# Performance work log

Hardware: AMD Instinct MI355X
Metric: run time of the kernel (lower is better)

## Reference

```python
import jax, jax.numpy as jnp
import numpy as np

B, H, W, C = 1, 56, 56, 96
DI = 192          # d_inner = ssm_ratio * hidden_dim
N  = 16           # d_state
DR = 6            # dt_rank = ceil(96/16)
K  = 4            # cross-scan directions
MH = 384          # mlp hidden = 4*C
L  = H * W


def _ln(x, g, b):
    m = x.mean(-1, keepdims=True)
    v = ((x - m) ** 2).mean(-1, keepdims=True)
    return (x - m) * jax.lax.rsqrt(v + 1e-5) * g + b


def setup_inputs() -> dict:
    key = jax.random.key(0)
    ks = jax.random.split(key, 12)
    r = lambda i, shape, s=0.02: jax.random.normal(ks[i], shape, jnp.float32) * s
    # S4D-real init for A_logs: log(1..N) tiled over K*DI channels
    A_logs = jnp.log(jnp.tile(jnp.arange(1, N + 1, dtype=jnp.float32)[None, :], (K * DI, 1)))
    return dict(
        x=jax.random.normal(ks[0], (B, H, W, C), jnp.float32),
        norm_g=jnp.ones((C,)), norm_b=jnp.zeros((C,)),
        in_proj_w=r(1, (C, 2 * DI)),
        conv_w=r(2, (3, 3, 1, DI)), conv_b=jnp.zeros((DI,)),
        x_proj_w=r(3, (K, DR + 2 * N, DI)),
        dt_projs_w=r(4, (K, DI, DR), 0.1), dt_projs_b=r(5, (K, DI), 0.1),
        A_logs=A_logs, Ds=jnp.ones((K * DI,)),
        out_norm_g=jnp.ones((DI,)), out_norm_b=jnp.zeros((DI,)),
        out_proj_w=r(6, (DI, C)),
        norm2_g=jnp.ones((C,)), norm2_b=jnp.zeros((C,)),
        fc1_w=r(7, (C, MH)), fc1_b=jnp.zeros((MH,)),
        fc2_w=r(8, (MH, C)), fc2_b=jnp.zeros((C,)),
    )


def _ss2d(x, in_proj_w, conv_w, conv_b, x_proj_w, dt_projs_w, dt_projs_b,
          A_logs, Ds, out_norm_g, out_norm_b, out_proj_w):
    xz = x @ in_proj_w                                  # (B,H,W,2*DI)
    xx, z = xz[..., :DI], xz[..., DI:]
    z = jax.nn.silu(z)
    xx = jax.lax.conv_general_dilated(
        xx, conv_w, (1, 1), 'SAME',
        dimension_numbers=('NHWC', 'HWIO', 'NHWC'),
        feature_group_count=DI) + conv_b               # depthwise 3x3
    xx = jax.nn.silu(xx)
    # cross-scan: row-major, col-major, and their reverses -> (B,K,DI,L)
    xd = jnp.transpose(xx, (0, 3, 1, 2)).reshape(B, DI, L)
    xt = jnp.transpose(xx, (0, 3, 2, 1)).reshape(B, DI, L)
    xs = jnp.stack([xd, xt, xd[..., ::-1], xt[..., ::-1]], 1)
    xdbl = jnp.einsum('bkdl,kcd->bkcl', xs, x_proj_w)
    dts, Bs, Cs = xdbl[:, :, :DR], xdbl[:, :, DR:DR + N], xdbl[:, :, DR + N:]
    dts = jnp.einsum('bkrl,kdr->bkdl', dts, dt_projs_w)
    dts = jax.nn.softplus(dts + dt_projs_b[None, :, :, None])      # (B,K,DI,L)
    A = -jnp.exp(A_logs).reshape(K, DI, N)
    # selective scan as first-order linear recurrence h_t = a_t*h_{t-1} + b_t
    a = jnp.exp(dts[..., None] * A[None, :, :, None, :])           # (B,K,DI,L,N)
    b = dts[..., None] * jnp.swapaxes(Bs, -1, -2)[:, :, None] * xs[..., None]
    def comb(c1, c2):
        a1, b1 = c1
        a2, b2 = c2
        return a1 * a2, a2 * b1 + b2
    _, hs = jax.lax.associative_scan(comb, (a, b), axis=3)         # (B,K,DI,L,N)
    ys = jnp.einsum('bkdln,bknl->bkdl', hs, Cs) + Ds.reshape(K, DI)[None, :, :, None] * xs
    # cross-merge: un-flip, un-transpose, sum the 4 directions
    yrow = ys[:, 0] + ys[:, 2, :, ::-1]
    ycol = ys[:, 1] + ys[:, 3, :, ::-1]
    y = yrow + jnp.transpose(ycol.reshape(B, DI, W, H), (0, 1, 3, 2)).reshape(B, DI, L)
    y = jnp.transpose(y.reshape(B, DI, H, W), (0, 2, 3, 1))        # (B,H,W,DI)
    y = _ln(y, out_norm_g, out_norm_b) * z
    return y @ out_proj_w


def reference(x, norm_g, norm_b, in_proj_w, conv_w, conv_b, x_proj_w,
              dt_projs_w, dt_projs_b, A_logs, Ds, out_norm_g, out_norm_b,
              out_proj_w, norm2_g, norm2_b, fc1_w, fc1_b, fc2_w, fc2_b):
    x = x + _ss2d(_ln(x, norm_g, norm_b), in_proj_w, conv_w, conv_b, x_proj_w,
                  dt_projs_w, dt_projs_b, A_logs, Ds, out_norm_g, out_norm_b, out_proj_w)
    h = _ln(x, norm2_g, norm2_b)
    x = x + (jax.nn.gelu(h @ fc1_w + fc1_b) @ fc2_w + fc2_b)
    return x
```

## Files before the change

### kernel.cpp

```cpp
#include <hip/hip_runtime.h>
#include <math.h>

constexpr int cH = 56, cW = 56, cC = 96, cDI = 192, cN = 16, cDR = 6, cK = 4, cMH = 384;
constexpr int cL = cH * cW;
constexpr int cNC = 49;
constexpr int cCH = 64;
constexpr float LOG2E = 1.44269504088896340736f;

__device__ __forceinline__ float fast_exp2(float x) { return __builtin_amdgcn_exp2f(x); }
__device__ __forceinline__ float siluf(float x) { return x / (1.f + expf(-x)); }
__device__ __forceinline__ float geluf(float x) {
    float x3 = x * x * x;
    return 0.5f * x * (1.f + tanhf(0.7978845608028654f * (x + 0.044715f * x3)));
}

__device__ __forceinline__ float dpp_red16(float v) {
    union { float f; int i; } u, r;
    u.f = v; r.i = __builtin_amdgcn_update_dpp(0, u.i, 0xB1, 0xF, 0xF, true);  v += r.f;
    u.f = v; r.i = __builtin_amdgcn_update_dpp(0, u.i, 0x4E, 0xF, 0xF, true);  v += r.f;
    u.f = v; r.i = __builtin_amdgcn_update_dpp(0, u.i, 0x141, 0xF, 0xF, true); v += r.f;
    u.f = v; r.i = __builtin_amdgcn_update_dpp(0, u.i, 0x140, 0xF, 0xF, true); v += r.f;
    return v;
}

__global__ void ln96_kernel(const float* __restrict__ x, const float* __restrict__ g,
                            const float* __restrict__ b, float* __restrict__ out, int M) {
    int wid = threadIdx.x >> 6;
    int lane = threadIdx.x & 63;
    int row = blockIdx.x * 4 + wid;
    if (row >= M) return;
    const float* xr = x + row * cC;
    float v0 = xr[lane];
    float v1 = (lane < cC - 64) ? xr[lane + 64] : 0.f;
    float s = v0 + v1;
    float sq = v0 * v0 + v1 * v1;
#pragma unroll
    for (int off = 32; off; off >>= 1) {
        s += __shfl_xor(s, off, 64);
        sq += __shfl_xor(sq, off, 64);
    }
    float m = s * (1.f / cC);
    float var = sq * (1.f / cC) - m * m;
    float rstd = rsqrtf(var + 1e-5f);
    out[row * cC + lane] = (v0 - m) * rstd * g[lane] + b[lane];
    if (lane < cC - 64)
        out[row * cC + lane + 64] = (v1 - m) * rstd * g[lane + 64] + b[lane + 64];
}

template <int ACT, bool HASB, bool HASR>
__global__ __launch_bounds__(256) void gemm_tile_kernel(
    const float* __restrict__ A, const float* __restrict__ B,
    const float* __restrict__ bias, const float* __restrict__ res,
    float* __restrict__ C, int M, int Nn, int Kk) {
    __shared__ float As[64][36];
    __shared__ float Bs[32][32];
    int tid = threadIdx.x;
    int tx = tid & 15;
    int ty = tid >> 4;
    int row0 = blockIdx.y * 64;
    int n0 = blockIdx.x * 32;
    float acc[4][2] = {{0.f, 0.f}, {0.f, 0.f}, {0.f, 0.f}, {0.f, 0.f}};
    int nt = Kk >> 5;
    for (int kt = 0; kt < nt; kt++) {
#pragma unroll
        for (int t = 0; t < 2; t++) {
            int f = tid + t * 256;
            int ar = f >> 3, ac = (f & 7) * 4;
            const float4 v = *reinterpret_cast<const float4*>(
                A + (size_t)(row0 + ar) * Kk + kt * 32 + ac);
            *reinterpret_cast<float4*>(&As[ar][ac]) = v;
        }
        {
            int br = tid >> 3, bc = (tid & 7) * 4;
            const float4 v = *reinterpret_cast<const float4*>(
                B + (size_t)(kt * 32 + br) * Nn + n0 + bc);
            *reinterpret_cast<float4*>(&Bs[br][bc]) = v;
        }
        __syncthreads();
#pragma unroll
        for (int k4 = 0; k4 < 8; k4++) {
            float4 a0 = *reinterpret_cast<float4*>(&As[ty * 4 + 0][k4 * 4]);
            float4 a1 = *reinterpret_cast<float4*>(&As[ty * 4 + 1][k4 * 4]);
            float4 a2 = *reinterpret_cast<float4*>(&As[ty * 4 + 2][k4 * 4]);
            float4 a3 = *reinterpret_cast<float4*>(&As[ty * 4 + 3][k4 * 4]);
            float2 b0 = *reinterpret_cast<float2*>(&Bs[k4 * 4 + 0][tx * 2]);
            float2 b1 = *reinterpret_cast<float2*>(&Bs[k4 * 4 + 1][tx * 2]);
            float2 b2 = *reinterpret_cast<float2*>(&Bs[k4 * 4 + 2][tx * 2]);
            float2 b3 = *reinterpret_cast<float2*>(&Bs[k4 * 4 + 3][tx * 2]);
            acc[0][0] = fmaf(a0.x, b0.x, acc[0][0]); acc[0][1] = fmaf(a0.x, b0.y, acc[0][1]);
            acc[1][0] = fmaf(a1.x, b0.x, acc[1][0]); acc[1][1] = fmaf(a1.x, b0.y, acc[1][1]);
            acc[2][0] = fmaf(a2.x, b0.x, acc[2][0]); acc[2][1] = fmaf(a2.x, b0.y, acc[2][1]);
            acc[3][0] = fmaf(a3.x, b0.x, acc[3][0]); acc[3][1] = fmaf(a3.x, b0.y, acc[3][1]);
            acc[0][0] = fmaf(a0.y, b1.x, acc[0][0]); acc[0][1] = fmaf(a0.y, b1.y, acc[0][1]);
            acc[1][0] = fmaf(a1.y, b1.x, acc[1][0]); acc[1][1] = fmaf(a1.y, b1.y, acc[1][1]);
            acc[2][0] = fmaf(a2.y, b1.x, acc[2][0]); acc[2][1] = fmaf(a2.y, b1.y, acc[2][1]);
            acc[3][0] = fmaf(a3.y, b1.x, acc[3][0]); acc[3][1] = fmaf(a3.y, b1.y, acc[3][1]);
            acc[0][0] = fmaf(a0.z, b2.x, acc[0][0]); acc[0][1] = fmaf(a0.z, b2.y, acc[0][1]);
            acc[1][0] = fmaf(a1.z, b2.x, acc[1][0]); acc[1][1] = fmaf(a1.z, b2.y, acc[1][1]);
            acc[2][0] = fmaf(a2.z, b2.x, acc[2][0]); acc[2][1] = fmaf(a2.z, b2.y, acc[2][1]);
            acc[3][0] = fmaf(a3.z, b2.x, acc[3][0]); acc[3][1] = fmaf(a3.z, b2.y, acc[3][1]);
            acc[0][0] = fmaf(a0.w, b3.x, acc[0][0]); acc[0][1] = fmaf(a0.w, b3.y, acc[0][1]);
            acc[1][0] = fmaf(a1.w, b3.x, acc[1][0]); acc[1][1] = fmaf(a1.w, b3.y, acc[1][1]);
            acc[2][0] = fmaf(a2.w, b3.x, acc[2][0]); acc[2][1] = fmaf(a2.w, b3.y, acc[2][1]);
            acc[3][0] = fmaf(a3.w, b3.x, acc[3][0]); acc[3][1] = fmaf(a3.w, b3.y, acc[3][1]);
        }
        __syncthreads();
    }
    int cc = n0 + tx * 2;
    float bx_ = 0.f, by_ = 0.f;
    if (HASB) { bx_ = bias[cc]; by_ = bias[cc + 1]; }
#pragma unroll
    for (int i = 0; i < 4; i++) {
        int rr = row0 + ty * 4 + i;
        float v0 = acc[i][0], v1 = acc[i][1];
        if (HASB) { v0 += bx_; v1 += by_; }
        if (ACT == 1) { v0 = geluf(v0); v1 = geluf(v1); }
        if (HASR) {
            const float2 r2 = *reinterpret_cast<const float2*>(res + (size_t)rr * Nn + cc);
            v0 += r2.x; v1 += r2.y;
        }
        float2 o; o.x = v0; o.y = v1;
        *reinterpret_cast<float2*>(C + (size_t)rr * Nn + cc) = o;
    }
}

__global__ void conv_silu_kernel(const float* __restrict__ xz, const float* __restrict__ cw,
                                 const float* __restrict__ cb, float* __restrict__ out) {
    int idx = blockIdx.x * 256 + threadIdx.x;
    if (idx >= cL * cDI) return;
    int d = idx % cDI;
    int l = idx / cDI;
    int h = l / cW, w = l % cW;
    float s = cb[d];
#pragma unroll
    for (int dh = 0; dh < 3; dh++) {
        int hh = h + dh - 1;
        if (hh < 0 || hh >= cH) continue;
#pragma unroll
        for (int dw = 0; dw < 3; dw++) {
            int w2 = w + dw - 1;
            if (w2 < 0 || w2 >= cW) continue;
            s = fmaf(xz[(size_t)(hh * cW + w2) * (2 * cDI) + d], cw[(dh * 3 + dw) * cDI + d], s);
        }
    }
    out[idx] = siluf(s);
}

__global__ void proj_kernel(const float* __restrict__ xconv, const float* __restrict__ xpw,
                            const float* __restrict__ dtw, const float* __restrict__ dtb,
                            float* __restrict__ dtout, float* __restrict__ Bsout,
                            float* __restrict__ Csout) {
    __shared__ float XS[16 * 193];
    __shared__ float DTS[6 * 16];
    int k = blockIdx.y;
    int p0 = blockIdx.x * 16;
    int tid = threadIdx.x;
    for (int idx = tid; idx < 16 * cDI; idx += 256) {
        int p = idx / cDI, d = idx % cDI;
        int j = p0 + p;
        int jj = (k >= 2) ? (cL - 1 - j) : j;
        int rrow = (k & 1) ? ((jj % cH) * cW + (jj / cH)) : jj;
        XS[p * 193 + d] = xconv[(size_t)rrow * cDI + d];
    }
    __syncthreads();
    for (int o = tid; o < 38 * 16; o += 256) {
        int c = o >> 4, p = o & 15;
        const float* wr = xpw + (size_t)(k * 38 + c) * cDI;
        const float* xr = XS + p * 193;
        float s = 0.f;
#pragma unroll 4
        for (int d = 0; d < cDI; d++) s = fmaf(wr[d], xr[d], s);
        if (c < 6) DTS[c * 16 + p] = s;
        else if (c < 22) Bsout[(size_t)(k * cL + p0 + p) * cN + (c - 6)] = s;
        else Csout[(size_t)(k * cL + p0 + p) * cN + (c - 22)] = s;
    }
    __syncthreads();
    for (int o = tid; o < cDI * 16; o += 256) {
        int d = o >> 4, p = o & 15;
        float s = dtb[k * cDI + d];
        const float* wr = dtw + (size_t)(k * cDI + d) * cDR;
#pragma unroll
        for (int r = 0; r < cDR; r++) s = fmaf(wr[r], DTS[r * 16 + p], s);
        float sp = (s > 20.f) ? s : log1pf(expf(s));
        dtout[(size_t)(k * cDI + d) * cL + p0 + p] = sp;
    }
}

__device__ __forceinline__ void walker_init(int k, int j0, int& r, int& dr) {
    if (k == 0) { r = j0; dr = 1; }
    else if (k == 1) { r = (j0 % cH) * cW + (j0 / cH); dr = cW; }
    else if (k == 2) { r = cL - 1 - j0; dr = -1; }
    else { int jp = cL - 1 - j0; r = (jp % cH) * cW + (jp / cH); dr = -cW; }
}
__device__ __forceinline__ void walker_step(int& r, int dr) {
    r += dr;
    if (r >= cL) r -= cL - 1;
    else if (r < 0) r += cL - 1;
}

__global__ void scan1_kernel(const float* __restrict__ dtbuf, const float* __restrict__ Bs,
                             const float* __restrict__ xconv, const float* __restrict__ Alogs,
                             float* __restrict__ carryP, float* __restrict__ carryH) {
    int bx = blockIdx.x;
    int c = bx % cNC;
    int t2 = bx / cNC;
    int d0 = (t2 % (cDI / 16)) * 16;
    int k = t2 / (cDI / 16);
    int g = threadIdx.x >> 4;
    int n = threadIdx.x & 15;
    int d = d0 + g;
    int kd = k * cDI + d;
    float An2 = -expf(Alogs[kd * cN + n]) * LOG2E;
    int j0 = c * cCH;
    int r, dr;
    walker_init(k, j0, r, dr);
    const float* dtp = dtbuf + (size_t)kd * cL;
    const float* bsp = Bs + (size_t)k * cL * cN + n;
    float h = 0.f, S = 0.f;
    for (int i = 0; i < cCH; i += 4) {
        int j = j0 + i;
        const float4 dt4 = *reinterpret_cast<const float4*>(dtp + j);
        float xv0 = xconv[r * cDI + d]; walker_step(r, dr);
        float xv1 = xconv[r * cDI + d]; walker_step(r, dr);
        float xv2 = xconv[r * cDI + d]; walker_step(r, dr);
        float xv3 = xconv[r * cDI + d]; walker_step(r, dr);
        float bv0 = bsp[(size_t)(j + 0) * cN];
        float bv1 = bsp[(size_t)(j + 1) * cN];
        float bv2 = bsp[(size_t)(j + 2) * cN];
        float bv3 = bsp[(size_t)(j + 3) * cN];
        float a0 = fast_exp2(An2 * dt4.x);
        float a1 = fast_exp2(An2 * dt4.y);
        float a2 = fast_exp2(An2 * dt4.z);
        float a3 = fast_exp2(An2 * dt4.w);
        h = fmaf(a0, h, dt4.x * bv0 * xv0);
        h = fmaf(a1, h, dt4.y * bv1 * xv1);
        h = fmaf(a2, h, dt4.z * bv2 * xv2);
        h = fmaf(a3, h, dt4.w * bv3 * xv3);
        S += dt4.x + dt4.y + dt4.z + dt4.w;
    }
    float P = fast_exp2(An2 * S);
    int idxc = (kd * cNC + c) * cN + n;
    carryH[idxc] = h;
    carryP[idxc] = P;
}

__global__ void scan2_kernel(const float* __restrict__ carryP, const float* __restrict__ carryH,
                             float* __restrict__ hin) {
    int gid = blockIdx.x * 256 + threadIdx.x;
    if (gid >= cK * cDI * cN) return;
    int kd = gid / cN, n = gid % cN;
    float h = 0.f;
    for (int c = 0; c < cNC; c++) {
        int idxc = (kd * cNC + c) * cN + n;
        hin[idxc] = h;
        h = fmaf(carryP[idxc], h, carryH[idxc]);
    }
}

__global__ void scan3_kernel(const float* __restrict__ dtbuf, const float* __restrict__ Bs,
                             const float* __restrict__ Cs, const float* __restrict__ xconv,
                             const float* __restrict__ Alogs, const float* __restrict__ Ds,
                             const float* __restrict__ hin, float* __restrict__ ysS) {
    int bx = blockIdx.x;
    int c = bx % cNC;
    int t2 = bx / cNC;
    int d0 = (t2 % (cDI / 16)) * 16;
    int k = t2 / (cDI / 16);
    int g = threadIdx.x >> 4;
    int n = threadIdx.x & 15;
    int d = d0 + g;
    int kd = k * cDI + d;
    float An2 = -expf(Alogs[kd * cN + n]) * LOG2E;
    float Dv = Ds[kd];
    int j0 = c * cCH;
    int r, dr;
    walker_init(k, j0, r, dr);
    const float* dtp = dtbuf + (size_t)kd * cL;
    const float* bsp = Bs + (size_t)k * cL * cN + n;
    const float* csp = Cs + (size_t)k * cL * cN + n;
    float h = hin[(kd * cNC + c) * cN + n];
    for (int i = 0; i < cCH; i += 4) {
        int j = j0 + i;
        const float4 dt4 = *reinterpret_cast<const float4*>(dtp + j);
        float xv0 = xconv[r * cDI + d]; walker_step(r, dr);
        float xv1 = xconv[r * cDI + d]; walker_step(r, dr);
        float xv2 = xconv[r * cDI + d]; walker_step(r, dr);
        float xv3 = xconv[r * cDI + d]; walker_step(r, dr);
        float bv0 = bsp[(size_t)(j + 0) * cN];
        float bv1 = bsp[(size_t)(j + 1) * cN];
        float bv2 = bsp[(size_t)(j + 2) * cN];
        float bv3 = bsp[(size_t)(j + 3) * cN];
        float cv0 = csp[(size_t)(j + 0) * cN];
        float cv1 = csp[(size_t)(j + 1) * cN];
        float cv2 = csp[(size_t)(j + 2) * cN];
        float cv3 = csp[(size_t)(j + 3) * cN];
        float a0 = fast_exp2(An2 * dt4.x);
        float a1 = fast_exp2(An2 * dt4.y);
        float a2 = fast_exp2(An2 * dt4.z);
        float a3 = fast_exp2(An2 * dt4.w);
        h = fmaf(a0, h, dt4.x * bv0 * xv0);
        float t0 = dpp_red16(h * cv0);
        h = fmaf(a1, h, dt4.y * bv1 * xv1);
        float t1 = dpp_red16(h * cv1);
        h = fmaf(a2, h, dt4.z * bv2 * xv2);
        float t2v = dpp_red16(h * cv2);
        h = fmaf(a3, h, dt4.w * bv3 * xv3);
        float t3 = dpp_red16(h * cv3);
        if (n == 0) {
            ysS[(size_t)(k * cL + j + 0) * cDI + d] = t0 + Dv * xv0;
            ysS[(size_t)(k * cL + j + 1) * cDI + d] = t1 + Dv * xv1;
            ysS[(size_t)(k * cL + j + 2) * cDI + d] = t2v + Dv * xv2;
            ysS[(size_t)(k * cL + j + 3) * cDI + d] = t3 + Dv * xv3;
        }
    }
}

__global__ void lnout_kernel(const float* __restrict__ ysS, const float* __restrict__ xz,
                             const float* __restrict__ g, const float* __restrict__ b,
                             float* __restrict__ ymul) {
    int wid = threadIdx.x >> 6, lane = threadIdx.x & 63;
    int l = blockIdx.x * 4 + wid;
    if (l >= cL) return;
    int h_ = l / cW, w_ = l % cW;
    int lc = w_ * cH + h_;
    float v[3];
    float s = 0.f, sq = 0.f;
#pragma unroll
    for (int j = 0; j < 3; j++) {
        int d = lane + j * 64;
        float t = ysS[(size_t)(0 * cL + l) * cDI + d] +
                  ysS[(size_t)(1 * cL + lc) * cDI + d] +
                  ysS[(size_t)(2 * cL + (cL - 1 - l)) * cDI + d] +
                  ysS[(size_t)(3 * cL + (cL - 1 - lc)) * cDI + d];
        v[j] = t;
        s += t;
        sq += t * t;
    }
#pragma unroll
    for (int off = 32; off; off >>= 1) {
        s += __shfl_xor(s, off, 64);
        sq += __shfl_xor(sq, off, 64);
    }
    float m = s * (1.f / cDI);
    float var = sq * (1.f / cDI) - m * m;
    float rstd = rsqrtf(var + 1e-5f);
#pragma unroll
    for (int j = 0; j < 3; j++) {
        int d = lane + j * 64;
        float z = xz[(size_t)l * (2 * cDI) + cDI + d];
        ymul[(size_t)l * cDI + d] = ((v[j] - m) * rstd * g[d] + b[d]) * siluf(z);
    }
}

extern "C" void kernel_launch(void* const* d_in, const int* in_sizes, int n_in,
                              void* d_out, int out_size, void* d_ws, size_t ws_size,
                              hipStream_t stream) {
    const float* x         = (const float*)d_in[0];
    const float* norm_g    = (const float*)d_in[1];
    const float* norm_b    = (const float*)d_in[2];
    const float* in_proj_w = (const float*)d_in[3];
    const float* conv_w    = (const float*)d_in[4];
    const float* conv_b    = (const float*)d_in[5];
    const float* x_proj_w  = (const float*)d_in[6];
    const float* dt_projs_w= (const float*)d_in[7];
    const float* dt_projs_b= (const float*)d_in[8];
    const float* A_logs    = (const float*)d_in[9];
    const float* Ds        = (const float*)d_in[10];
    const float* out_norm_g= (const float*)d_in[11];
    const float* out_norm_b= (const float*)d_in[12];
    const float* out_proj_w= (const float*)d_in[13];
    const float* norm2_g   = (const float*)d_in[14];
    const float* norm2_b   = (const float*)d_in[15];
    const float* fc1_w     = (const float*)d_in[16];
    const float* fc1_b     = (const float*)d_in[17];
    const float* fc2_w     = (const float*)d_in[18];
    const float* fc2_b     = (const float*)d_in[19];

    float* ws = (float*)d_ws;
    float* ln_buf = ws;
    float* xz     = ws + 301056;
    float* xconv  = ws + 1505280;
    float* dtb_   = ws + 2107392;
    float* Bs     = ws + 4515840;
    float* Cs     = ws + 4716544;
    float* hin    = ws + 4917248;
    float* ysS    = ws + 5519360;
    float* cP     = ysS;
    float* cHh    = ysS + 602112;
    float* ymul   = xconv;
    float* x1     = ws + 7927808;
    float* hm     = xz;
    float* out    = (float*)d_out;

    ln96_kernel<<<cL / 4, 256, 0, stream>>>(x, norm_g, norm_b, ln_buf, cL);
    gemm_tile_kernel<0, false, false><<<dim3(384 / 32, cL / 64), 256, 0, stream>>>(
        ln_buf, in_proj_w, nullptr, nullptr, xz, cL, 2 * cDI, cC);
    conv_silu_kernel<<<(cL * cDI) / 256, 256, 0, stream>>>(xz, conv_w, conv_b, xconv);
    proj_kernel<<<dim3(cL / 16, cK), 256, 0, stream>>>(xconv, x_proj_w, dt_projs_w,
                                                       dt_projs_b, dtb_, Bs, Cs);
    scan1_kernel<<<cK * (cDI / 16) * cNC, 256, 0, stream>>>(dtb_, Bs, xconv, A_logs, cP, cHh);
    scan2_kernel<<<(cK * cDI * cN + 255) / 256, 256, 0, stream>>>(cP, cHh, hin);
    scan3_kernel<<<cK * (cDI / 16) * cNC, 256, 0, stream>>>(dtb_, Bs, Cs, xconv, A_logs, Ds,
                                                            hin, ysS);
    lnout_kernel<<<cL / 4, 256, 0, stream>>>(ysS, xz, out_norm_g, out_norm_b, ymul);
    gemm_tile_kernel<0, false, true><<<dim3(96 / 32, cL / 64), 256, 0, stream>>>(
        ymul, out_proj_w, nullptr, x, x1, cL, cC, cDI);
    ln96_kernel<<<cL / 4, 256, 0, stream>>>(x1, norm2_g, norm2_b, ln_buf, cL);
    gemm_tile_kernel<1, true, false><<<dim3(384 / 32, cL / 64), 256, 0, stream>>>(
        ln_buf, fc1_w, fc1_b, nullptr, hm, cL, cMH, cC);
    gemm_tile_kernel<0, true, true><<<dim3(96 / 32, cL / 64), 256, 0, stream>>>(
        hm, fc2_w, fc2_b, x1, out, cL, cC, cMH);
}
```

Before: 162.4 us.

## Restructure selective scan to one thread per channel with all states in registers

The scan kernels change from 16 lanes per channel (one per state, with a DPP reduction over C) to one thread per channel that keeps all 16 states in registers and accumulates y locally. B and C per chunk are staged in shared memory, dt is stored transposed (position-major) so loads across channels coalesce, and dt_projs weights are cached in LDS in proj_kernel. Chunk length drops from 64 to 16, giving 196 chunks so the grid stays large, at the cost of a longer sequential carry pass in scan2 and larger carry buffers. The workspace is re-laid out so the carry buffers no longer alias ysS.

```diff
diff --git a/kernel.cpp b/kernel.cpp
--- a/kernel.cpp
+++ b/kernel.cpp
@@ -3,8 +3,8 @@
 
 constexpr int cH = 56, cW = 56, cC = 96, cDI = 192, cN = 16, cDR = 6, cK = 4, cMH = 384;
 constexpr int cL = cH * cW;
-constexpr int cNC = 49;
-constexpr int cCH = 64;
+constexpr int cNC = 196;
+constexpr int cCH = 16;
 constexpr float LOG2E = 1.44269504088896340736f;
 
 __device__ __forceinline__ float fast_exp2(float x) { return __builtin_amdgcn_exp2f(x); }
@@ -12,15 +12,6 @@
 __device__ __forceinline__ float geluf(float x) {
     float x3 = x * x * x;
     return 0.5f * x * (1.f + tanhf(0.7978845608028654f * (x + 0.044715f * x3)));
-}
-
-__device__ __forceinline__ float dpp_red16(float v) {
-    union { float f; int i; } u, r;
-    u.f = v; r.i = __builtin_amdgcn_update_dpp(0, u.i, 0xB1, 0xF, 0xF, true);  v += r.f;
-    u.f = v; r.i = __builtin_amdgcn_update_dpp(0, u.i, 0x4E, 0xF, 0xF, true);  v += r.f;
-    u.f = v; r.i = __builtin_amdgcn_update_dpp(0, u.i, 0x141, 0xF, 0xF, true); v += r.f;
-    u.f = v; r.i = __builtin_amdgcn_update_dpp(0, u.i, 0x140, 0xF, 0xF, true); v += r.f;
-    return v;
 }
 
 __global__ void ln96_kernel(const float* __restrict__ x, const float* __restrict__ g,
@@ -148,13 +139,15 @@
 
 __global__ void proj_kernel(const float* __restrict__ xconv, const float* __restrict__ xpw,
                             const float* __restrict__ dtw, const float* __restrict__ dtb,
-                            float* __restrict__ dtout, float* __restrict__ Bsout,
+                            float* __restrict__ dtT, float* __restrict__ Bsout,
                             float* __restrict__ Csout) {
     __shared__ float XS[16 * 193];
     __shared__ float DTS[6 * 16];
+    __shared__ float DTW[cDI * cDR];
     int k = blockIdx.y;
     int p0 = blockIdx.x * 16;
     int tid = threadIdx.x;
+    for (int i = tid; i < cDI * cDR; i += 256) DTW[i] = dtw[k * cDI * cDR + i];
     for (int idx = tid; idx < 16 * cDI; idx += 256) {
         int p = idx / cDI, d = idx % cDI;
         int j = p0 + p;
@@ -176,13 +169,12 @@
     }
     __syncthreads();
     for (int o = tid; o < cDI * 16; o += 256) {
-        int d = o >> 4, p = o & 15;
+        int d = o % cDI, p = o / cDI;
         float s = dtb[k * cDI + d];
-        const float* wr = dtw + (size_t)(k * cDI + d) * cDR;
-#pragma unroll
-        for (int r = 0; r < cDR; r++) s = fmaf(wr[r], DTS[r * 16 + p], s);
+#pragma unroll
+        for (int r = 0; r < cDR; r++) s = fmaf(DTW[d * cDR + r], DTS[r * 16 + p], s);
         float sp = (s > 20.f) ? s : log1pf(expf(s));
-        dtout[(size_t)(k * cDI + d) * cL + p0 + p] = sp;
+        dtT[(size_t)(k * cL + p0 + p) * cDI + d] = sp;
     }
 }
 
@@ -198,50 +190,54 @@
     else if (r < 0) r += cL - 1;
 }
 
-__global__ void scan1_kernel(const float* __restrict__ dtbuf, const float* __restrict__ Bs,
-                             const float* __restrict__ xconv, const float* __restrict__ Alogs,
-                             float* __restrict__ carryP, float* __restrict__ carryH) {
-    int bx = blockIdx.x;
-    int c = bx % cNC;
-    int t2 = bx / cNC;
-    int d0 = (t2 % (cDI / 16)) * 16;
-    int k = t2 / (cDI / 16);
-    int g = threadIdx.x >> 4;
-    int n = threadIdx.x & 15;
-    int d = d0 + g;
+__global__ __launch_bounds__(192) void scan1_kernel(
+    const float* __restrict__ dtT, const float* __restrict__ Bs,
+    const float* __restrict__ xconv, const float* __restrict__ Alogs,
+    float* __restrict__ carryP, float* __restrict__ carryH) {
+    int c = blockIdx.x % cNC;
+    int k = blockIdx.x / cNC;
+    int d = threadIdx.x;
     int kd = k * cDI + d;
-    float An2 = -expf(Alogs[kd * cN + n]) * LOG2E;
     int j0 = c * cCH;
+    __shared__ float BS[cCH * cN];
+    for (int i = threadIdx.x; i < cCH * cN; i += 192)
+        BS[i] = Bs[(size_t)(k * cL + j0) * cN + i];
+    float An2[cN];
+#pragma unroll
+    for (int n = 0; n < cN; n++)
+        An2[n] = -fast_exp2(Alogs[kd * cN + n] * LOG2E) * LOG2E;
     int r, dr;
     walker_init(k, j0, r, dr);
-    const float* dtp = dtbuf + (size_t)kd * cL;
-    const float* bsp = Bs + (size_t)k * cL * cN + n;
-    float h = 0.f, S = 0.f;
-    for (int i = 0; i < cCH; i += 4) {
-        int j = j0 + i;
-        const float4 dt4 = *reinterpret_cast<const float4*>(dtp + j);
-        float xv0 = xconv[r * cDI + d]; walker_step(r, dr);
-        float xv1 = xconv[r * cDI + d]; walker_step(r, dr);
-        float xv2 = xconv[r * cDI + d]; walker_step(r, dr);
-        float xv3 = xconv[r * cDI + d]; walker_step(r, dr);
-        float bv0 = bsp[(size_t)(j + 0) * cN];
-        float bv1 = bsp[(size_t)(j + 1) * cN];
-        float bv2 = bsp[(size_t)(j + 2) * cN];
-        float bv3 = bsp[(size_t)(j + 3) * cN];
-        float a0 = fast_exp2(An2 * dt4.x);
-        float a1 = fast_exp2(An2 * dt4.y);
-        float a2 = fast_exp2(An2 * dt4.z);
-        float a3 = fast_exp2(An2 * dt4.w);
-        h = fmaf(a0, h, dt4.x * bv0 * xv0);
-        h = fmaf(a1, h, dt4.y * bv1 * xv1);
-        h = fmaf(a2, h, dt4.z * bv2 * xv2);
-        h = fmaf(a3, h, dt4.w * bv3 * xv3);
-        S += dt4.x + dt4.y + dt4.z + dt4.w;
-    }
-    float P = fast_exp2(An2 * S);
-    int idxc = (kd * cNC + c) * cN + n;
-    carryH[idxc] = h;
-    carryP[idxc] = P;
+    __syncthreads();
+    float h[cN];
+#pragma unroll
+    for (int n = 0; n < cN; n++) h[n] = 0.f;
+    float S = 0.f;
+    const float* dtp = dtT + (size_t)(k * cL + j0) * cDI + d;
+    for (int i = 0; i < cCH; i++) {
+        float dt = dtp[(size_t)i * cDI];
+        float xv = xconv[r * cDI + d];
+        walker_step(r, dr);
+        float dtx = dt * xv;
+        S += dt;
+        const float4 b0 = *reinterpret_cast<const float4*>(&BS[i * cN + 0]);
+        const float4 b1 = *reinterpret_cast<const float4*>(&BS[i * cN + 4]);
+        const float4 b2 = *reinterpret_cast<const float4*>(&BS[i * cN + 8]);
+        const float4 b3 = *reinterpret_cast<const float4*>(&BS[i * cN + 12]);
+        float bb[cN] = {b0.x, b0.y, b0.z, b0.w, b1.x, b1.y, b1.z, b1.w,
+                        b2.x, b2.y, b2.z, b2.w, b3.x, b3.y, b3.z, b3.w};
+#pragma unroll
+        for (int n = 0; n < cN; n++) {
+            float a = fast_exp2(An2[n] * dt);
+            h[n] = fmaf(a, h[n], bb[n] * dtx);
+        }
+    }
+    size_t cb = (size_t)(kd * cNC + c) * cN;
+#pragma unroll
+    for (int n = 0; n < cN; n++) {
+        carryH[cb + n] = h[n];
+        carryP[cb + n] = fast_exp2(An2[n] * S);
+    }
 }
 
 __global__ void scan2_kernel(const float* __restrict__ carryP, const float* __restrict__ carryH,
@@ -251,67 +247,76 @@
     int kd = gid / cN, n = gid % cN;
     float h = 0.f;
     for (int c = 0; c < cNC; c++) {
-        int idxc = (kd * cNC + c) * cN + n;
+        size_t idxc = (size_t)(kd * cNC + c) * cN + n;
         hin[idxc] = h;
         h = fmaf(carryP[idxc], h, carryH[idxc]);
     }
 }
 
-__global__ void scan3_kernel(const float* __restrict__ dtbuf, const float* __restrict__ Bs,
-                             const float* __restrict__ Cs, const float* __restrict__ xconv,
-                             const float* __restrict__ Alogs, const float* __restrict__ Ds,
-                             const float* __restrict__ hin, float* __restrict__ ysS) {
-    int bx = blockIdx.x;
-    int c = bx % cNC;
-    int t2 = bx / cNC;
-    int d0 = (t2 % (cDI / 16)) * 16;
-    int k = t2 / (cDI / 16);
-    int g = threadIdx.x >> 4;
-    int n = threadIdx.x & 15;
-    int d = d0 + g;
+__global__ __launch_bounds__(192) void scan3_kernel(
+    const float* __restrict__ dtT, const float* __restrict__ Bs,
+    const float* __restrict__ Cs, const float* __restrict__ xconv,
+    const float* __restrict__ Alogs, const float* __restrict__ Ds,
+    const float* __restrict__ hin, float* __restrict__ ysS) {
+    int c = blockIdx.x % cNC;
+    int k = blockIdx.x / cNC;
+    int d = threadIdx.x;
     int kd = k * cDI + d;
-    float An2 = -expf(Alogs[kd * cN + n]) * LOG2E;
+    int j0 = c * cCH;
+    __shared__ float BS[cCH * cN];
+    __shared__ float CS[cCH * cN];
+    for (int i = threadIdx.x; i < cCH * cN; i += 192) {
+        BS[i] = Bs[(size_t)(k * cL + j0) * cN + i];
+        CS[i] = Cs[(size_t)(k * cL + j0) * cN + i];
+    }
+    float An2[cN];
+#pragma unroll
+    for (int n = 0; n < cN; n++)
+        An2[n] = -fast_exp2(Alogs[kd * cN + n] * LOG2E) * LOG2E;
     float Dv = Ds[kd];
-    int j0 = c * cCH;
     int r, dr;
     walker_init(k, j0, r, dr);
-    const float* dtp = dtbuf + (size_t)kd * cL;
-    const float* bsp = Bs + (size_t)k * cL * cN + n;
-    const float* csp = Cs + (size_t)k * cL * cN + n;
-    float h = hin[(kd * cNC + c) * cN + n];
-    for (int i = 0; i < cCH; i += 4) {
-        int j = j0 + i;
-        const float4 dt4 = *reinterpret_cast<const float4*>(dtp + j);
-        float xv0 = xconv[r * cDI + d]; walker_step(r, dr);
-        float xv1 = xconv[r * cDI + d]; walker_step(r, dr);
-        float xv2 = xconv[r * cDI + d]; walker_step(r, dr);
-        float xv3 = xconv[r * cDI + d]; walker_step(r, dr);
-        float bv0 = bsp[(size_t)(j + 0) * cN];
-        float bv1 = bsp[(size_t)(j + 1) * cN];
-        float bv2 = bsp[(size_t)(j + 2) * cN];
-        float bv3 = bsp[(size_t)(j + 3) * cN];
-        float cv0 = csp[(size_t)(j + 0) * cN];
-        float cv1 = csp[(size_t)(j + 1) * cN];
-        float cv2 = csp[(size_t)(j + 2) * cN];
-        float cv3 = csp[(size_t)(j + 3) * cN];
-        float a0 = fast_exp2(An2 * dt4.x);
-        float a1 = fast_exp2(An2 * dt4.y);
-        float a2 = fast_exp2(An2 * dt4.z);
-        float a3 = fast_exp2(An2 * dt4.w);
-        h = fmaf(a0, h, dt4.x * bv0 * xv0);
-        float t0 = dpp_red16(h * cv0);
-        h = fmaf(a1, h, dt4.y * bv1 * xv1);
-        float t1 = dpp_red16(h * cv1);
-        h = fmaf(a2, h, dt4.z * bv2 * xv2);
-        float t2v = dpp_red16(h * cv2);
-        h = fmaf(a3, h, dt4.w * bv3 * xv3);
-        float t3 = dpp_red16(h * cv3);
-        if (n == 0) {
-            ysS[(size_t)(k * cL + j + 0) * cDI + d] = t0 + Dv * xv0;
-            ysS[(size_t)(k * cL + j + 1) * cDI + d] = t1 + Dv * xv1;
-            ysS[(size_t)(k * cL + j + 2) * cDI + d] = t2v + Dv * xv2;
-            ysS[(size_t)(k * cL + j + 3) * cDI + d] = t3 + Dv * xv3;
-        }
+    float h[cN];
+    size_t cb = (size_t)(kd * cNC + c) * cN;
+#pragma unroll
+    for (int n = 0; n < cN; n++) h[n] = hin[cb + n];
+    __syncthreads();
+    const float* dtp = dtT + (size_t)(k * cL + j0) * cDI + d;
+    float* yp = ysS + (size_t)(k * cL + j0) * cDI + d;
+    for (int i = 0; i < cCH; i++) {
+        float dt = dtp[(size_t)i * cDI];
+        float xv = xconv[r * cDI + d];
+        walker_step(r, dr);
+        float dtx = dt * xv;
+        const float4 b0 = *reinterpret_cast<const float4*>(&BS[i * cN + 0]);
+        const float4 b1 = *reinterpret_cast<const float4*>(&BS[i * cN + 4]);
+        const float4 b2 = *reinterpret_cast<const float4*>(&BS[i * cN + 8]);
+        const float4 b3 = *reinterpret_cast<const float4*>(&BS[i * cN + 12]);
+        float bb[cN] = {b0.x, b0.y, b0.z, b0.w, b1.x, b1.y, b1.z, b1.w,
+                        b2.x, b2.y, b2.z, b2.w, b3.x, b3.y, b3.z, b3.w};
+        const float4 c0 = *reinterpret_cast<const float4*>(&CS[i * cN + 0]);
+        const float4 c1 = *reinterpret_cast<const float4*>(&CS[i * cN + 4]);
+        const float4 c2 = *reinterpret_cast<const float4*>(&CS[i * cN + 8]);
+        const float4 c3 = *reinterpret_cast<const float4*>(&CS[i * cN + 12]);
+        float cc[cN] = {c0.x, c0.y, c0.z, c0.w, c1.x, c1.y, c1.z, c1.w,
+                        c2.x, c2.y, c2.z, c2.w, c3.x, c3.y, c3.z, c3.w};
+        float y0 = 0.f, y1 = 0.f, y2 = 0.f, y3 = 0.f;
+#pragma unroll
+        for (int n = 0; n < cN; n += 4) {
+            float a0 = fast_exp2(An2[n + 0] * dt);
+            float a1 = fast_exp2(An2[n + 1] * dt);
+            float a2 = fast_exp2(An2[n + 2] * dt);
+            float a3 = fast_exp2(An2[n + 3] * dt);
+            h[n + 0] = fmaf(a0, h[n + 0], bb[n + 0] * dtx);
+            h[n + 1] = fmaf(a1, h[n + 1], bb[n + 1] * dtx);
+            h[n + 2] = fmaf(a2, h[n + 2], bb[n + 2] * dtx);
+            h[n + 3] = fmaf(a3, h[n + 3], bb[n + 3] * dtx);
+            y0 = fmaf(h[n + 0], cc[n + 0], y0);
+            y1 = fmaf(h[n + 1], cc[n + 1], y1);
+            y2 = fmaf(h[n + 2], cc[n + 2], y2);
+            y3 = fmaf(h[n + 3], cc[n + 3], y3);
+        }
+        yp[(size_t)i * cDI] = (y0 + y1) + (y2 + y3) + Dv * xv;
     }
 }
 
@@ -380,15 +385,15 @@
     float* ln_buf = ws;
     float* xz     = ws + 301056;
     float* xconv  = ws + 1505280;
-    float* dtb_   = ws + 2107392;
+    float* dtT    = ws + 2107392;
     float* Bs     = ws + 4515840;
     float* Cs     = ws + 4716544;
     float* hin    = ws + 4917248;
-    float* ysS    = ws + 5519360;
-    float* cP     = ysS;
-    float* cHh    = ysS + 602112;
+    float* cP     = ws + 7325696;
+    float* cHh    = ws + 9734144;
+    float* ysS    = ws + 12142592;
+    float* x1     = ws + 14551040;
     float* ymul   = xconv;
-    float* x1     = ws + 7927808;
     float* hm     = xz;
     float* out    = (float*)d_out;
 
@@ -397,11 +402,10 @@
         ln_buf, in_proj_w, nullptr, nullptr, xz, cL, 2 * cDI, cC);
     conv_silu_kernel<<<(cL * cDI) / 256, 256, 0, stream>>>(xz, conv_w, conv_b, xconv);
     proj_kernel<<<dim3(cL / 16, cK), 256, 0, stream>>>(xconv, x_proj_w, dt_projs_w,
-                                                       dt_projs_b, dtb_, Bs, Cs);
-    scan1_kernel<<<cK * (cDI / 16) * cNC, 256, 0, stream>>>(dtb_, Bs, xconv, A_logs, cP, cHh);
+                                                       dt_projs_b, dtT, Bs, Cs);
+    scan1_kernel<<<cK * cNC, 192, 0, stream>>>(dtT, Bs, xconv, A_logs, cP, cHh);
     scan2_kernel<<<(cK * cDI * cN + 255) / 256, 256, 0, stream>>>(cP, cHh, hin);
-    scan3_kernel<<<cK * (cDI / 16) * cNC, 256, 0, stream>>>(dtb_, Bs, Cs, xconv, A_logs, Ds,
-                                                            hin, ysS);
+    scan3_kernel<<<cK * cNC, 192, 0, stream>>>(dtT, Bs, Cs, xconv, A_logs, Ds, hin, ysS);
     lnout_kernel<<<cL / 4, 256, 0, stream>>>(ysS, xz, out_norm_g, out_norm_b, ymul);
     gemm_tile_kernel<0, false, true><<<dim3(96 / 32, cL / 64), 256, 0, stream>>>(
         ymul, out_proj_w, nullptr, x, x1, cL, cC, cDI);
```

Result: slower. 166.8 us (+2.8%).
